# Kernel optimization log

Measured on AMD Instinct MI355X. Metric: run time of the kernel, lower is better.

The kernel has to match this reference:

```python
import jax, jax.numpy as jnp
import numpy as np

USER_NUM = 100000
ITEM_NUM = 100000
N = USER_NUM + ITEM_NUM
E = 3200000
D_INT = 64
D_GEO = 64
L = 3  # layer_num


def setup_inputs() -> dict:
    key = jax.random.key(0)
    k0, k1, k2, k3, k4 = jax.random.split(key, 5)
    return {
        "user_int": jax.random.normal(k0, (USER_NUM, D_INT), dtype=jnp.float32) * 0.01,
        "item_int": jax.random.normal(k1, (ITEM_NUM, D_INT), dtype=jnp.float32) * 0.01,
        "user_geo": jax.random.normal(k2, (USER_NUM, D_GEO), dtype=jnp.float32) * 0.01,
        "item_geo": jax.random.normal(k3, (ITEM_NUM, D_GEO), dtype=jnp.float32) * 0.01,
        "edge_index": jax.random.randint(k4, (2, E), 0, N, dtype=jnp.int32),
    }


def _lgconv(x, src, dst, norm):
    # LGConv: out[dst] += norm * x[src]  (symmetric gcn_norm, no self-loops)
    msg = x[src] * norm[:, None]  # [E, d]
    return jax.ops.segment_sum(msg, dst, num_segments=N)


def reference(user_int, item_int, user_geo, item_geo, edge_index):
    src = edge_index[0]
    dst = edge_index[1]
    # gcn_norm with add_self_loops=False: deg over destination (col) nodes
    deg = jax.ops.segment_sum(jnp.ones(src.shape[0], jnp.float32), dst, num_segments=N)
    dis = jnp.where(deg > 0, jax.lax.rsqrt(jnp.where(deg > 0, deg, 1.0)), 0.0)
    norm = dis[src] * dis[dst]  # [E]

    def run(emb0):
        acc = emb0
        emb = emb0
        for _ in range(L):
            emb = _lgconv(emb, src, dst, norm)
            acc = acc + emb
        # 1/(L+1) * mean over (L+1) stacked embeddings == sum / (L+1)^2
        return acc / float((L + 1) ** 2)

    int_res = run(jnp.concatenate([user_int, item_int], axis=0))
    geo_res = run(jnp.concatenate([user_geo, item_geo], axis=0))
    return (int_res[:USER_NUM], int_res[USER_NUM:],
            geo_res[:USER_NUM], geo_res[USER_NUM:])
```

## Files before the change

### kernel.cpp

```cpp
#include <hip/hip_runtime.h>
#include <hip/hip_fp16.h>

#define USER_N 100000
#define ITEM_N 100000
#define NODE_N (USER_N + ITEM_N)
#define D 64
#define INV_SCALE (1.0f / 16.0f)
#define ELL_MAX 64
#define BUILD_BLOCKS 2048

__global__ void build_kernel(const int* __restrict__ src, const int* __restrict__ dst,
                             int* __restrict__ deg, int* __restrict__ col_ell, int E,
                             const float* __restrict__ user_int, const float* __restrict__ item_int,
                             const float* __restrict__ user_geo, const float* __restrict__ item_geo,
                             __half* __restrict__ x0h) {
    int tid = blockIdx.x * blockDim.x + threadIdx.x;
    const int T = BUILD_BLOCKS * 256;
    const int ICH = NODE_N * 16;
    const int M = (E > ICH) ? E : ICH;
    for (int k = tid; k < M; k += T) {
        if (k < E) {
            int t = dst[k];
            int s = src[k];
            int slot = atomicAdd(&deg[t], 1);
            if (slot < ELL_MAX)
                col_ell[((size_t)t << 6) + slot] = s;
        }
        if (k < ICH) {
            int n = k >> 4;
            int m = k & 15;
            const float* base = (m < 8)
                ? ((n < USER_N) ? user_int + (size_t)n * 64 : item_int + (size_t)(n - USER_N) * 64)
                : ((n < USER_N) ? user_geo + (size_t)n * 64 : item_geo + (size_t)(n - USER_N) * 64);
            int f0 = (m & 7) * 8;
            float4 a = *(const float4*)(base + f0);
            float4 b = *(const float4*)(base + f0 + 4);
            __half2 o[4];
            o[0] = __float22half2_rn(make_float2(a.x, a.y));
            o[1] = __float22half2_rn(make_float2(a.z, a.w));
            o[2] = __float22half2_rn(make_float2(b.x, b.y));
            o[3] = __float22half2_rn(make_float2(b.z, b.w));
            *(uint4*)(x0h + (((size_t)n) << 7) + (m << 3)) = *(const uint4*)o;
        }
    }
}

__global__ void dis_kernel(const int* __restrict__ deg, float* __restrict__ dis) {
    int i = blockIdx.x * blockDim.x + threadIdx.x;
    if (i < NODE_N) {
        int d = deg[i];
        dis[i] = d > 0 ? rsqrtf((float)d) : 0.0f;
    }
}


#define RED2(v) { v += __shfl_xor(v, 16); v += __shfl_xor(v, 32); }

template <bool WEIGHTED>
__global__ void gather_ell_kernel(const int* __restrict__ deg, const int* __restrict__ col_ell,
                                  const float* __restrict__ dis,
                                  const __half* __restrict__ Yc, __half* __restrict__ Yn) {
    int wid = (int)((blockIdx.x * blockDim.x + threadIdx.x) >> 6);
    int lane = threadIdx.x & 63;
    int sub = lane >> 4;
    int ch  = lane & 15;
    if (wid >= NODE_N) return;
    int cnt = deg[wid];
    if (cnt > ELL_MAX) cnt = ELL_MAX;
    const int* row = col_ell + ((size_t)wid << 6);
    float a0x = 0, a0y = 0, a1x = 0, a1y = 0, a2x = 0, a2y = 0, a3x = 0, a3y = 0;
    for (int e0 = 0; e0 < cnt; e0 += 4) {
        int e = e0 + sub;
        uint4 r = make_uint4(0, 0, 0, 0);
        float w = 0.0f;
        if (e < cnt) {
            int s = row[e];
            w = WEIGHTED ? dis[s] : 1.0f;
            r = *(const uint4*)(Yc + (((size_t)s) << 7) + (ch << 3));
        }
        const __half2* h = reinterpret_cast<const __half2*>(&r);
        float2 f0 = __half22float2(h[0]);
        float2 f1 = __half22float2(h[1]);
        float2 f2 = __half22float2(h[2]);
        float2 f3 = __half22float2(h[3]);
        if (WEIGHTED) {
            a0x += w * f0.x; a0y += w * f0.y; a1x += w * f1.x; a1y += w * f1.y;
            a2x += w * f2.x; a2y += w * f2.y; a3x += w * f3.x; a3y += w * f3.y;
        } else {
            a0x += f0.x; a0y += f0.y; a1x += f1.x; a1y += f1.y;
            a2x += f2.x; a2y += f2.y; a3x += f3.x; a3y += f3.y;
        }
    }
    RED2(a0x) RED2(a0y) RED2(a1x) RED2(a1y)
    RED2(a2x) RED2(a2y) RED2(a3x) RED2(a3y)
    if (lane < 16) {
        float d = dis[wid];
        float d2 = d * d;
        __half2 o[4];
        o[0] = __float22half2_rn(make_float2(a0x * d2, a0y * d2));
        o[1] = __float22half2_rn(make_float2(a1x * d2, a1y * d2));
        o[2] = __float22half2_rn(make_float2(a2x * d2, a2y * d2));
        o[3] = __float22half2_rn(make_float2(a3x * d2, a3y * d2));
        *(uint4*)(Yn + (((size_t)wid) << 7) + (ch << 3)) = *(const uint4*)o;
    }
}

__global__ void gather_last_ell_kernel(const int* __restrict__ deg, const int* __restrict__ col_ell,
                                       const float* __restrict__ dis,
                                       const __half* __restrict__ x0h, const __half* __restrict__ y1,
                                       const __half* __restrict__ y2, float* __restrict__ out) {
    int wid = (int)((blockIdx.x * blockDim.x + threadIdx.x) >> 6);
    int lane = threadIdx.x & 63;
    int sub = lane >> 4;
    int ch  = lane & 15;
    if (wid >= NODE_N) return;
    int dg = deg[wid];
    int cnt = dg > ELL_MAX ? ELL_MAX : dg;
    const int* row = col_ell + ((size_t)wid << 6);
    float a0x = 0, a0y = 0, a1x = 0, a1y = 0, a2x = 0, a2y = 0, a3x = 0, a3y = 0;
    for (int e0 = 0; e0 < cnt; e0 += 4) {
        int e = e0 + sub;
        uint4 r = make_uint4(0, 0, 0, 0);
        if (e < cnt) {
            int s = row[e];
            r = *(const uint4*)(y2 + (((size_t)s) << 7) + (ch << 3));
        }
        const __half2* h = reinterpret_cast<const __half2*>(&r);
        float2 f0 = __half22float2(h[0]);
        float2 f1 = __half22float2(h[1]);
        float2 f2 = __half22float2(h[2]);
        float2 f3 = __half22float2(h[3]);
        a0x += f0.x; a0y += f0.y; a1x += f1.x; a1y += f1.y;
        a2x += f2.x; a2y += f2.y; a3x += f3.x; a3y += f3.y;
    }
    RED2(a0x) RED2(a0y) RED2(a1x) RED2(a1y)
    RED2(a2x) RED2(a2y) RED2(a3x) RED2(a3y)
    if (lane < 16) {
        float S[8] = {a0x, a0y, a1x, a1y, a2x, a2y, a3x, a3y};
        float d = dis[wid];
        float sd = dg > 0 ? sqrtf((float)dg) : 0.0f;
        size_t rbase = (((size_t)wid) << 7) + (ch << 3);
        uint4 r0 = *(const uint4*)(x0h + rbase);
        uint4 r1 = *(const uint4*)(y1 + rbase);
        uint4 r2 = *(const uint4*)(y2 + rbase);
        const __half2* h0 = reinterpret_cast<const __half2*>(&r0);
        const __half2* h1 = reinterpret_cast<const __half2*>(&r1);
        const __half2* h2 = reinterpret_cast<const __half2*>(&r2);
        float res[8];
#pragma unroll
        for (int k = 0; k < 4; ++k) {
            float2 f0 = __half22float2(h0[k]);
            float2 f1 = __half22float2(h1[k]);
            float2 f2 = __half22float2(h2[k]);
            res[2 * k]     = (f0.x + (f1.x + f2.x) * sd + S[2 * k] * d) * INV_SCALE;
            res[2 * k + 1] = (f0.y + (f1.y + f2.y) * sd + S[2 * k + 1] * d) * INV_SCALE;
        }
        size_t off = (ch < 8) ? ((size_t)wid * 64 + (size_t)ch * 8)
                              : ((size_t)NODE_N * 64 + (size_t)wid * 64 + (size_t)(ch - 8) * 8);
        *(float4*)(out + off)     = make_float4(res[0], res[1], res[2], res[3]);
        *(float4*)(out + off + 4) = make_float4(res[4], res[5], res[6], res[7]);
    }
}


__global__ void deg_only_kernel(const int* __restrict__ dst, int* __restrict__ deg, int E) {
    int i = blockIdx.x * blockDim.x + threadIdx.x;
    int stride = gridDim.x * blockDim.x;
    for (; i < E; i += stride)
        atomicAdd(&deg[dst[i]], 1);
}

__global__ void init_kernel(const float* __restrict__ user, const float* __restrict__ item,
                            float* __restrict__ X, float* __restrict__ out) {
    int i = blockIdx.x * blockDim.x + threadIdx.x;
    int stride = gridDim.x * blockDim.x;
    const int total = NODE_N * D;
    for (; i < total; i += stride) {
        float v = (i < USER_N * D) ? user[i] : item[i - USER_N * D];
        X[i] = v;
        out[i] = v * INV_SCALE;
    }
}

__global__ void scatter_kernel(const int* __restrict__ src, const int* __restrict__ dst,
                               const float* __restrict__ dis,
                               const float* __restrict__ Xc, float* __restrict__ Xn, int E) {
    int wid  = (blockIdx.x * blockDim.x + threadIdx.x) >> 6;
    int lane = threadIdx.x & 63;
    int nw   = (gridDim.x * blockDim.x) >> 6;
    for (int e = wid; e < E; e += nw) {
        int s = src[e];
        int t = dst[e];
        float nrm = dis[s] * dis[t];
        if (nrm != 0.0f) {
            float v = Xc[(size_t)s * D + lane] * nrm;
            atomicAdd(&Xn[(size_t)t * D + lane], v);
        }
    }
}

__global__ void accum_kernel(const float* __restrict__ Xn, float* __restrict__ out) {
    int i = blockIdx.x * blockDim.x + threadIdx.x;
    int stride = gridDim.x * blockDim.x;
    const int total = NODE_N * D;
    for (; i < total; i += stride)
        out[i] += Xn[i] * INV_SCALE;
}


static inline size_t align256(size_t x) { return (x + 255) & ~(size_t)255; }

extern "C" void kernel_launch(void* const* d_in, const int* in_sizes, int n_in,
                              void* d_out, int out_size, void* d_ws, size_t ws_size,
                              hipStream_t stream) {
    const float* user_int = (const float*)d_in[0];
    const float* item_int = (const float*)d_in[1];
    const float* user_geo = (const float*)d_in[2];
    const float* item_geo = (const float*)d_in[3];
    const int*   edge     = (const int*)d_in[4];
    const int E = in_sizes[4] / 2;
    const int* srcv = edge;
    const int* dstv = edge + E;
    float* out = (float*)d_out;

    char* ws = (char*)d_ws;
    size_t off = 0;
    int* deg_i = (int*)(ws + off);        off = align256(off + (size_t)NODE_N * 4);
    float* dis = (float*)(ws + off);      off = align256(off + (size_t)NODE_N * 4);
    size_t head = off;
    int* col_ell = (int*)(ws + off);      off = align256(off + (size_t)NODE_N * ELL_MAX * 4);
    __half* x0h = (__half*)(ws + off);    off = align256(off + (size_t)NODE_N * 128 * 2);
    __half* y1 = (__half*)(ws + off);     off = align256(off + (size_t)NODE_N * 128 * 2);
    __half* y2 = (__half*)(ws + off);     off = align256(off + (size_t)NODE_N * 128 * 2);
    const size_t FULL_NEED = off;

    hipMemsetAsync(deg_i, 0, (size_t)NODE_N * 4, stream);

    if (ws_size >= FULL_NEED) {
        build_kernel<<<BUILD_BLOCKS, 256, 0, stream>>>(
            srcv, dstv, deg_i, col_ell, E,
            user_int, item_int, user_geo, item_geo, x0h);
        dis_kernel<<<(NODE_N + 255) / 256, 256, 0, stream>>>(deg_i, dis);

        const int gblocks = (NODE_N + 3) / 4;
        gather_ell_kernel<true ><<<gblocks, 256, 0, stream>>>(deg_i, col_ell, dis, x0h, y1);
        gather_ell_kernel<false><<<gblocks, 256, 0, stream>>>(deg_i, col_ell, dis, y1, y2);
        gather_last_ell_kernel<<<gblocks, 256, 0, stream>>>(deg_i, col_ell, dis, x0h, y1, y2, out);
    } else {
        deg_only_kernel<<<4096, 256, 0, stream>>>(dstv, deg_i, E);
        dis_kernel<<<(NODE_N + 255) / 256, 256, 0, stream>>>(deg_i, dis);
        float* Fa = (float*)(ws + head);
        float* Fb = Fa + (size_t)NODE_N * D;
        const size_t xbytes = (size_t)NODE_N * D * sizeof(float);
        for (int e = 0; e < 2; ++e) {
            const float* u  = (e == 0) ? user_int : user_geo;
            const float* it = (e == 0) ? item_int : item_geo;
            float* o = out + (size_t)e * NODE_N * D;
            init_kernel<<<4096, 256, 0, stream>>>(u, it, Fa, o);
            float* cur = Fa;
            float* nxt = Fb;
            for (int l = 0; l < 3; ++l) {
                hipMemsetAsync(nxt, 0, xbytes, stream);
                scatter_kernel<<<8192, 256, 0, stream>>>(srcv, dstv, dis, cur, nxt, E);
                accum_kernel<<<4096, 256, 0, stream>>>(nxt, o);
                float* t = cur; cur = nxt; nxt = t;
            }
        }
    }
}
```

Baseline: 590.1 us.

## Process two nodes per wavefront with batched loads and drop the dis kernel

Each gather wavefront now handles two destination nodes and issues eight independent row loads per iteration, covering 16 edges per node per step, to raise memory-level parallelism. The separate dis kernel is removed: the rsqrt of degree is computed inline from deg in the gathers. The build kernel loop is unrolled by four so more atomics and loads are in flight. In exchange, register pressure rises, lanes idle when the two nodes' degrees differ, and the extra deg lookups per neighbour replace the single dis lookup.

```diff
diff --git a/kernel.cpp b/kernel.cpp
--- a/kernel.cpp
+++ b/kernel.cpp
@@ -18,30 +18,41 @@
     const int T = BUILD_BLOCKS * 256;
     const int ICH = NODE_N * 16;
     const int M = (E > ICH) ? E : ICH;
-    for (int k = tid; k < M; k += T) {
-        if (k < E) {
-            int t = dst[k];
-            int s = src[k];
-            int slot = atomicAdd(&deg[t], 1);
-            if (slot < ELL_MAX)
-                col_ell[((size_t)t << 6) + slot] = s;
-        }
-        if (k < ICH) {
-            int n = k >> 4;
-            int m = k & 15;
-            const float* base = (m < 8)
-                ? ((n < USER_N) ? user_int + (size_t)n * 64 : item_int + (size_t)(n - USER_N) * 64)
-                : ((n < USER_N) ? user_geo + (size_t)n * 64 : item_geo + (size_t)(n - USER_N) * 64);
-            int f0 = (m & 7) * 8;
-            float4 a = *(const float4*)(base + f0);
-            float4 b = *(const float4*)(base + f0 + 4);
-            __half2 o[4];
-            o[0] = __float22half2_rn(make_float2(a.x, a.y));
-            o[1] = __float22half2_rn(make_float2(a.z, a.w));
-            o[2] = __float22half2_rn(make_float2(b.x, b.y));
-            o[3] = __float22half2_rn(make_float2(b.z, b.w));
-            *(uint4*)(x0h + (((size_t)n) << 7) + (m << 3)) = *(const uint4*)o;
-        }
+
+    auto edge_op = [&](int k) {
+        int t = dst[k];
+        int s = src[k];
+        int slot = atomicAdd(&deg[t], 1);
+        if (slot < ELL_MAX)
+            col_ell[((size_t)t << 6) + slot] = s;
+    };
+    auto init_op = [&](int k) {
+        int n = k >> 4;
+        int m = k & 15;
+        const float* base = (m < 8)
+            ? ((n < USER_N) ? user_int + (size_t)n * 64 : item_int + (size_t)(n - USER_N) * 64)
+            : ((n < USER_N) ? user_geo + (size_t)n * 64 : item_geo + (size_t)(n - USER_N) * 64);
+        int f0 = (m & 7) * 8;
+        float4 a = *(const float4*)(base + f0);
+        float4 b = *(const float4*)(base + f0 + 4);
+        __half2 o[4];
+        o[0] = __float22half2_rn(make_float2(a.x, a.y));
+        o[1] = __float22half2_rn(make_float2(a.z, a.w));
+        o[2] = __float22half2_rn(make_float2(b.x, b.y));
+        o[3] = __float22half2_rn(make_float2(b.z, b.w));
+        *(uint4*)(x0h + (((size_t)n) << 7) + (m << 3)) = *(const uint4*)o;
+    };
+
+    for (int k = tid; k < M; k += 4 * T) {
+        int k1 = k + T, k2 = k + 2 * T, k3 = k + 3 * T;
+        if (k  < E) edge_op(k);
+        if (k1 < E) edge_op(k1);
+        if (k2 < E) edge_op(k2);
+        if (k3 < E) edge_op(k3);
+        if (k  < ICH) init_op(k);
+        if (k1 < ICH) init_op(k1);
+        if (k2 < ICH) init_op(k2);
+        if (k3 < ICH) init_op(k3);
     }
 }
 
@@ -56,109 +67,150 @@
 
 #define RED2(v) { v += __shfl_xor(v, 16); v += __shfl_xor(v, 32); }
 
+#define DECL_ACC(P) float P##0x=0,P##0y=0,P##1x=0,P##1y=0,P##2x=0,P##2y=0,P##3x=0,P##3y=0;
+#define ACC4P(P, r, w) { \
+    const __half2* h_ = reinterpret_cast<const __half2*>(&(r)); \
+    float2 g0 = __half22float2(h_[0]); \
+    float2 g1 = __half22float2(h_[1]); \
+    float2 g2 = __half22float2(h_[2]); \
+    float2 g3 = __half22float2(h_[3]); \
+    P##0x += (w) * g0.x; P##0y += (w) * g0.y; P##1x += (w) * g1.x; P##1y += (w) * g1.y; \
+    P##2x += (w) * g2.x; P##2y += (w) * g2.y; P##3x += (w) * g3.x; P##3y += (w) * g3.y; }
+#define RED_ALL(P) RED2(P##0x) RED2(P##0y) RED2(P##1x) RED2(P##1y) \
+                   RED2(P##2x) RED2(P##2y) RED2(P##3x) RED2(P##3y)
+
+__device__ __forceinline__ float wdis(const int* deg, int s) {
+    int d = deg[s];
+    return d > 0 ? rsqrtf((float)d) : 0.0f;
+}
+
 template <bool WEIGHTED>
-__global__ void gather_ell_kernel(const int* __restrict__ deg, const int* __restrict__ col_ell,
-                                  const float* __restrict__ dis,
-                                  const __half* __restrict__ Yc, __half* __restrict__ Yn) {
-    int wid = (int)((blockIdx.x * blockDim.x + threadIdx.x) >> 6);
+__global__ void gather2_kernel(const int* __restrict__ deg, const int* __restrict__ col_ell,
+                               const __half* __restrict__ Yc, __half* __restrict__ Yn) {
+    int wv = (int)((blockIdx.x * blockDim.x + threadIdx.x) >> 6);
     int lane = threadIdx.x & 63;
     int sub = lane >> 4;
     int ch  = lane & 15;
-    if (wid >= NODE_N) return;
-    int cnt = deg[wid];
-    if (cnt > ELL_MAX) cnt = ELL_MAX;
-    const int* row = col_ell + ((size_t)wid << 6);
-    float a0x = 0, a0y = 0, a1x = 0, a1y = 0, a2x = 0, a2y = 0, a3x = 0, a3y = 0;
-    for (int e0 = 0; e0 < cnt; e0 += 4) {
-        int e = e0 + sub;
-        uint4 r = make_uint4(0, 0, 0, 0);
-        float w = 0.0f;
-        if (e < cnt) {
-            int s = row[e];
-            w = WEIGHTED ? dis[s] : 1.0f;
-            r = *(const uint4*)(Yc + (((size_t)s) << 7) + (ch << 3));
-        }
-        const __half2* h = reinterpret_cast<const __half2*>(&r);
-        float2 f0 = __half22float2(h[0]);
-        float2 f1 = __half22float2(h[1]);
-        float2 f2 = __half22float2(h[2]);
-        float2 f3 = __half22float2(h[3]);
-        if (WEIGHTED) {
-            a0x += w * f0.x; a0y += w * f0.y; a1x += w * f1.x; a1y += w * f1.y;
-            a2x += w * f2.x; a2y += w * f2.y; a3x += w * f3.x; a3y += w * f3.y;
-        } else {
-            a0x += f0.x; a0y += f0.y; a1x += f1.x; a1y += f1.y;
-            a2x += f2.x; a2y += f2.y; a3x += f3.x; a3y += f3.y;
-        }
-    }
-    RED2(a0x) RED2(a0y) RED2(a1x) RED2(a1y)
-    RED2(a2x) RED2(a2y) RED2(a3x) RED2(a3y)
+    int n0 = wv * 2;
+    if (n0 >= NODE_N) return;
+    int n1 = n0 + 1;
+    int d0 = deg[n0], d1 = deg[n1];
+    int c0 = d0 > ELL_MAX ? ELL_MAX : d0;
+    int c1 = d1 > ELL_MAX ? ELL_MAX : d1;
+    const int* r0 = col_ell + ((size_t)n0 << 6);
+    const int* r1 = col_ell + ((size_t)n1 << 6);
+    DECL_ACC(A) DECL_ACC(B)
+    int cm = c0 > c1 ? c0 : c1;
+    for (int e0 = 0; e0 < cm; e0 += 16) {
+        int s[8]; float w[8];
+#pragma unroll
+        for (int g = 0; g < 4; ++g) {
+            int e = e0 + g * 4 + sub;
+            bool va = e < c0, vb = e < c1;
+            s[g]     = va ? r0[e] : 0;
+            s[4 + g] = vb ? r1[e] : 0;
+            w[g]     = va ? (WEIGHTED ? wdis(deg, s[g])     : 1.0f) : 0.0f;
+            w[4 + g] = vb ? (WEIGHTED ? wdis(deg, s[4 + g]) : 1.0f) : 0.0f;
+        }
+        uint4 r[8];
+#pragma unroll
+        for (int j = 0; j < 8; ++j)
+            r[j] = *(const uint4*)(Yc + (((size_t)s[j]) << 7) + (ch << 3));
+#pragma unroll
+        for (int g = 0; g < 4; ++g) {
+            ACC4P(A, r[g], w[g])
+            ACC4P(B, r[4 + g], w[4 + g])
+        }
+    }
+    RED_ALL(A) RED_ALL(B)
     if (lane < 16) {
-        float d = dis[wid];
-        float d2 = d * d;
-        __half2 o[4];
-        o[0] = __float22half2_rn(make_float2(a0x * d2, a0y * d2));
-        o[1] = __float22half2_rn(make_float2(a1x * d2, a1y * d2));
-        o[2] = __float22half2_rn(make_float2(a2x * d2, a2y * d2));
-        o[3] = __float22half2_rn(make_float2(a3x * d2, a3y * d2));
-        *(uint4*)(Yn + (((size_t)wid) << 7) + (ch << 3)) = *(const uint4*)o;
-    }
-}
-
-__global__ void gather_last_ell_kernel(const int* __restrict__ deg, const int* __restrict__ col_ell,
-                                       const float* __restrict__ dis,
-                                       const __half* __restrict__ x0h, const __half* __restrict__ y1,
-                                       const __half* __restrict__ y2, float* __restrict__ out) {
-    int wid = (int)((blockIdx.x * blockDim.x + threadIdx.x) >> 6);
+        float da = d0 > 0 ? rsqrtf((float)d0) : 0.0f;
+        float db = d1 > 0 ? rsqrtf((float)d1) : 0.0f;
+        float da2 = da * da, db2 = db * db;
+        __half2 oa[4], ob[4];
+        oa[0] = __float22half2_rn(make_float2(A0x * da2, A0y * da2));
+        oa[1] = __float22half2_rn(make_float2(A1x * da2, A1y * da2));
+        oa[2] = __float22half2_rn(make_float2(A2x * da2, A2y * da2));
+        oa[3] = __float22half2_rn(make_float2(A3x * da2, A3y * da2));
+        ob[0] = __float22half2_rn(make_float2(B0x * db2, B0y * db2));
+        ob[1] = __float22half2_rn(make_float2(B1x * db2, B1y * db2));
+        ob[2] = __float22half2_rn(make_float2(B2x * db2, B2y * db2));
+        ob[3] = __float22half2_rn(make_float2(B3x * db2, B3y * db2));
+        *(uint4*)(Yn + (((size_t)n0) << 7) + (ch << 3)) = *(const uint4*)oa;
+        *(uint4*)(Yn + (((size_t)n1) << 7) + (ch << 3)) = *(const uint4*)ob;
+    }
+}
+
+__global__ void gather_last2_kernel(const int* __restrict__ deg, const int* __restrict__ col_ell,
+                                    const __half* __restrict__ x0h, const __half* __restrict__ y1,
+                                    const __half* __restrict__ y2, float* __restrict__ out) {
+    int wv = (int)((blockIdx.x * blockDim.x + threadIdx.x) >> 6);
     int lane = threadIdx.x & 63;
     int sub = lane >> 4;
     int ch  = lane & 15;
-    if (wid >= NODE_N) return;
-    int dg = deg[wid];
-    int cnt = dg > ELL_MAX ? ELL_MAX : dg;
-    const int* row = col_ell + ((size_t)wid << 6);
-    float a0x = 0, a0y = 0, a1x = 0, a1y = 0, a2x = 0, a2y = 0, a3x = 0, a3y = 0;
-    for (int e0 = 0; e0 < cnt; e0 += 4) {
-        int e = e0 + sub;
-        uint4 r = make_uint4(0, 0, 0, 0);
-        if (e < cnt) {
-            int s = row[e];
-            r = *(const uint4*)(y2 + (((size_t)s) << 7) + (ch << 3));
-        }
-        const __half2* h = reinterpret_cast<const __half2*>(&r);
-        float2 f0 = __half22float2(h[0]);
-        float2 f1 = __half22float2(h[1]);
-        float2 f2 = __half22float2(h[2]);
-        float2 f3 = __half22float2(h[3]);
-        a0x += f0.x; a0y += f0.y; a1x += f1.x; a1y += f1.y;
-        a2x += f2.x; a2y += f2.y; a3x += f3.x; a3y += f3.y;
-    }
-    RED2(a0x) RED2(a0y) RED2(a1x) RED2(a1y)
-    RED2(a2x) RED2(a2y) RED2(a3x) RED2(a3y)
+    int n0 = wv * 2;
+    if (n0 >= NODE_N) return;
+    int n1 = n0 + 1;
+    int d0 = deg[n0], d1 = deg[n1];
+    int c0 = d0 > ELL_MAX ? ELL_MAX : d0;
+    int c1 = d1 > ELL_MAX ? ELL_MAX : d1;
+    const int* r0 = col_ell + ((size_t)n0 << 6);
+    const int* r1 = col_ell + ((size_t)n1 << 6);
+    DECL_ACC(A) DECL_ACC(B)
+    int cm = c0 > c1 ? c0 : c1;
+    for (int e0 = 0; e0 < cm; e0 += 16) {
+        int s[8]; float w[8];
+#pragma unroll
+        for (int g = 0; g < 4; ++g) {
+            int e = e0 + g * 4 + sub;
+            bool va = e < c0, vb = e < c1;
+            s[g]     = va ? r0[e] : 0;
+            s[4 + g] = vb ? r1[e] : 0;
+            w[g]     = va ? 1.0f : 0.0f;
+            w[4 + g] = vb ? 1.0f : 0.0f;
+        }
+        uint4 r[8];
+#pragma unroll
+        for (int j = 0; j < 8; ++j)
+            r[j] = *(const uint4*)(y2 + (((size_t)s[j]) << 7) + (ch << 3));
+#pragma unroll
+        for (int g = 0; g < 4; ++g) {
+            ACC4P(A, r[g], w[g])
+            ACC4P(B, r[4 + g], w[4 + g])
+        }
+    }
+    RED_ALL(A) RED_ALL(B)
     if (lane < 16) {
-        float S[8] = {a0x, a0y, a1x, a1y, a2x, a2y, a3x, a3y};
-        float d = dis[wid];
-        float sd = dg > 0 ? sqrtf((float)dg) : 0.0f;
-        size_t rbase = (((size_t)wid) << 7) + (ch << 3);
-        uint4 r0 = *(const uint4*)(x0h + rbase);
-        uint4 r1 = *(const uint4*)(y1 + rbase);
-        uint4 r2 = *(const uint4*)(y2 + rbase);
-        const __half2* h0 = reinterpret_cast<const __half2*>(&r0);
-        const __half2* h1 = reinterpret_cast<const __half2*>(&r1);
-        const __half2* h2 = reinterpret_cast<const __half2*>(&r2);
-        float res[8];
-#pragma unroll
-        for (int k = 0; k < 4; ++k) {
-            float2 f0 = __half22float2(h0[k]);
-            float2 f1 = __half22float2(h1[k]);
-            float2 f2 = __half22float2(h2[k]);
-            res[2 * k]     = (f0.x + (f1.x + f2.x) * sd + S[2 * k] * d) * INV_SCALE;
-            res[2 * k + 1] = (f0.y + (f1.y + f2.y) * sd + S[2 * k + 1] * d) * INV_SCALE;
-        }
-        size_t off = (ch < 8) ? ((size_t)wid * 64 + (size_t)ch * 8)
-                              : ((size_t)NODE_N * 64 + (size_t)wid * 64 + (size_t)(ch - 8) * 8);
-        *(float4*)(out + off)     = make_float4(res[0], res[1], res[2], res[3]);
-        *(float4*)(out + off + 4) = make_float4(res[4], res[5], res[6], res[7]);
+        float SA[8] = {A0x, A0y, A1x, A1y, A2x, A2y, A3x, A3y};
+        float SB[8] = {B0x, B0y, B1x, B1y, B2x, B2y, B3x, B3y};
+#pragma unroll
+        for (int p = 0; p < 2; ++p) {
+            int n = p == 0 ? n0 : n1;
+            int dg = p == 0 ? d0 : d1;
+            const float* S = p == 0 ? SA : SB;
+            float d = dg > 0 ? rsqrtf((float)dg) : 0.0f;
+            float sd = dg > 0 ? sqrtf((float)dg) : 0.0f;
+            size_t rbase = (((size_t)n) << 7) + (ch << 3);
+            uint4 q0 = *(const uint4*)(x0h + rbase);
+            uint4 q1 = *(const uint4*)(y1 + rbase);
+            uint4 q2 = *(const uint4*)(y2 + rbase);
+            const __half2* h0 = reinterpret_cast<const __half2*>(&q0);
+            const __half2* h1 = reinterpret_cast<const __half2*>(&q1);
+            const __half2* h2 = reinterpret_cast<const __half2*>(&q2);
+            float res[8];
+#pragma unroll
+            for (int k = 0; k < 4; ++k) {
+                float2 f0 = __half22float2(h0[k]);
+                float2 f1 = __half22float2(h1[k]);
+                float2 f2 = __half22float2(h2[k]);
+                res[2 * k]     = (f0.x + (f1.x + f2.x) * sd + S[2 * k] * d) * INV_SCALE;
+                res[2 * k + 1] = (f0.y + (f1.y + f2.y) * sd + S[2 * k + 1] * d) * INV_SCALE;
+            }
+            size_t off = (ch < 8) ? ((size_t)n * 64 + (size_t)ch * 8)
+                                  : ((size_t)NODE_N * 64 + (size_t)n * 64 + (size_t)(ch - 8) * 8);
+            *(float4*)(out + off)     = make_float4(res[0], res[1], res[2], res[3]);
+            *(float4*)(out + off + 4) = make_float4(res[4], res[5], res[6], res[7]);
+        }
     }
 }
 
@@ -240,12 +292,11 @@
         build_kernel<<<BUILD_BLOCKS, 256, 0, stream>>>(
             srcv, dstv, deg_i, col_ell, E,
             user_int, item_int, user_geo, item_geo, x0h);
-        dis_kernel<<<(NODE_N + 255) / 256, 256, 0, stream>>>(deg_i, dis);
-
-        const int gblocks = (NODE_N + 3) / 4;
-        gather_ell_kernel<true ><<<gblocks, 256, 0, stream>>>(deg_i, col_ell, dis, x0h, y1);
-        gather_ell_kernel<false><<<gblocks, 256, 0, stream>>>(deg_i, col_ell, dis, y1, y2);
-        gather_last_ell_kernel<<<gblocks, 256, 0, stream>>>(deg_i, col_ell, dis, x0h, y1, y2, out);
+
+        const int gblocks = (NODE_N / 2 + 3) / 4;
+        gather2_kernel<true ><<<gblocks, 256, 0, stream>>>(deg_i, col_ell, x0h, y1);
+        gather2_kernel<false><<<gblocks, 256, 0, stream>>>(deg_i, col_ell, y1, y2);
+        gather_last2_kernel<<<gblocks, 256, 0, stream>>>(deg_i, col_ell, x0h, y1, y2, out);
     } else {
         deg_only_kernel<<<4096, 256, 0, stream>>>(dstv, deg_i, E);
         dis_kernel<<<(NODE_N + 255) / 256, 256, 0, stream>>>(deg_i, dis);
```

After: 619.8 us. +5.0%, slower.
